# Kernel optimization log

Hardware: AMD Instinct MI355X
Metric: run time of the kernel (lower is better)

The kernel has to match this reference:

```python
import jax, jax.numpy as jnp
import numpy as np

B, I, O, ORDER = 16384, 256, 256, 8
LO, HI = -1.0, 1.0


def setup_inputs() -> dict:
    key = jax.random.key(0)
    k1, k2, k3 = jax.random.split(key, 3)
    x = jax.random.normal(k1, (B, I), dtype=jnp.float32)
    weights = jax.random.normal(k2, (O, I), dtype=jnp.float32)
    # BernsteinBasisFunction init: randn(order+1) * 0.1, one per (o, i) pair
    coeffs = jax.random.normal(k3, (O, I, ORDER + 1), dtype=jnp.float32) * 0.1
    return {"x": x, "weights": weights, "coeffs": coeffs}


def reference(x, weights, coeffs):
    # x: [B, I]; weights: [O, I]; coeffs: [O, I, K+1]
    K = coeffs.shape[-1] - 1
    zoom = (HI - LO) / 2.0
    pan = (HI + LO) / 2.0
    xt = jnp.tanh(x) * zoom + pan          # squash into [LO, HI]
    x_a = xt - LO                          # [B, I]
    x_b = HI - xt                          # [B, I]
    e = jnp.arange(K + 1)
    # ber[b, i, k] = x_a^k * x_b^(K-k)  (unnormalized Bernstein basis)
    ber = (x_a[..., None] ** e) * (x_b[..., None] ** (K - e))  # [B, I, K+1]
    # transformed[b, o, i] = sum_k coeffs[o,i,k] * ber[b,i,k]; out = einsum('boi,oi->bo')
    # Fused: fold weights into coeffs to avoid the [B, O, I] intermediate.
    wc = coeffs * weights[..., None]       # [O, I, K+1]
    return jnp.einsum('bik,oik->bo', ber, wc)
```

## Files before the change

kernel.cpp:

```cpp
#include <hip/hip_runtime.h>
#include <hip/hip_bf16.h>


#define BDIM 16384
#define IDIM 256
#define ODIM 256
#define NK 9
#define NCHUNK 4
#define NSTEP 36
#define STEP_ELEMS (ODIM * 64)
#define CGW 4

typedef short short8 __attribute__((ext_vector_type(8)));
typedef float floatx4 __attribute__((ext_vector_type(4)));

__global__ __launch_bounds__(256) void prep_wc2(const float* __restrict__ weights,
                                                const float* __restrict__ coeffs,
                                                ushort* __restrict__ wc) {
    int idx  = blockIdx.x * 256 + threadIdx.x;
    int step = idx >> 11;
    int c    = idx & 2047;
    int big    = c >> 6;
    int lane_w = c & 63;
    int o    = (big >> 1) * 16 + (lane_w & 15);
    int s    = big & 1;
    int quad = lane_w >> 4;
    int ic = step / 9;
    int k  = step - ic * 9;
    int i0 = ic * 64 + s * 32 + quad * 8;

    const float* cp = coeffs + (size_t)(o * IDIM + i0) * NK + k;
    float4 w0 = *(const float4*)(weights + o * IDIM + i0);
    float4 w1 = *(const float4*)(weights + o * IDIM + i0 + 4);
    float wv[8] = {w0.x, w0.y, w0.z, w0.w, w1.x, w1.y, w1.z, w1.w};

    union { ushort us[8]; int4 v; __hip_bfloat162 h2[4]; } pk;
#pragma unroll
    for (int j = 0; j < 8; j += 2) {
        float a = cp[(size_t)j * NK] * wv[j];
        float b = cp[(size_t)(j + 1) * NK] * wv[j + 1];
        pk.h2[j >> 1] = __float22bfloat162_rn(make_float2(a, b));
    }
    *(int4*)(wc + (size_t)step * STEP_ELEMS + (size_t)c * 8) = pk.v;
}

__global__ __launch_bounds__(512, 2) void bern_gemm(const float* __restrict__ x,
                                                    const ushort* __restrict__ wc,
                                                    float* __restrict__ out) {
    __shared__ ushort Blds[2][16384];

    const int tid  = threadIdx.x;
    const int wave = tid >> 6;
    const int lane = tid & 63;
    const int cg   = blockIdx.x & 3;
    const int rb   = (blockIdx.x >> 2) * 256 + wave * 32;
    const int lrow = lane & 15;
    const int jseg = (lane >> 4) * 8;

    float p[2][2][8];
    float r[2][2][8];
    floatx4 acc[2][4];
    floatx4 zero = {0.0f, 0.0f, 0.0f, 0.0f};
#pragma unroll
    for (int m = 0; m < 2; ++m)
#pragma unroll
        for (int n = 0; n < 4; ++n)
            acc[m][n] = zero;

#define LOAD_X(ic_)                                                             \
    {                                                                           \
        _Pragma("unroll") for (int m = 0; m < 2; ++m)                           \
        _Pragma("unroll") for (int s = 0; s < 2; ++s) {                         \
            const float* xp = x + (size_t)(rb + m * 16 + lrow) * IDIM           \
                              + (ic_) * 64 + s * 32 + jseg;                     \
            float4 v0 = *(const float4*)(xp);                                   \
            float4 v1 = *(const float4*)(xp + 4);                               \
            p[m][s][0] = v0.x; p[m][s][1] = v0.y;                               \
            p[m][s][2] = v0.z; p[m][s][3] = v0.w;                               \
            p[m][s][4] = v1.x; p[m][s][5] = v1.y;                               \
            p[m][s][6] = v1.z; p[m][s][7] = v1.w;                               \
        }                                                                       \
    }

#define SETUP_BASIS()                                                           \
    {                                                                           \
        _Pragma("unroll") for (int m = 0; m < 2; ++m)                           \
        _Pragma("unroll") for (int s = 0; s < 2; ++s)                           \
        _Pragma("unroll") for (int e = 0; e < 8; ++e) {                         \
            float t  = __builtin_amdgcn_exp2f(p[m][s][e] * 2.8853900817779268f);\
            float q  = 2.0f * __builtin_amdgcn_rcpf(t + 1.0f);                  \
            float q2 = q * q;                                                   \
            float q4 = q2 * q2;                                                 \
            p[m][s][e] = q4 * q4;                                               \
            r[m][s][e] = t;                                                     \
        }                                                                       \
    }

#define STAGE(g_, b_)                                                           \
    {                                                                           \
        _Pragma("unroll") for (int q = 0; q < 4; ++q) {                         \
            int st  = (g_) * 4 + q;                                             \
            const ushort* sp = wc + (size_t)st * STEP_ELEMS + cg * 4096         \
                               + wave * 512 + lane * 8;                         \
            ushort* dp = &Blds[b_][(q * 8 + wave) * 512 + lane * 8];            \
            __builtin_amdgcn_global_load_lds(                                   \
                (const __attribute__((address_space(1))) void*)sp,              \
                (__attribute__((address_space(3))) void*)dp, 16, 0, 0);         \
        }                                                                       \
    }

    LOAD_X(0);
    SETUP_BASIS();
    STAGE(0, 0);

#pragma unroll
    for (int g = 0; g < 9; ++g) {
        __syncthreads();
        if (g < 8) STAGE(g + 1, (g + 1) & 1);

#pragma unroll
        for (int k4 = 0; k4 < 4; ++k4) {
            const int step = g * 4 + k4;
            if (step == 9 || step == 18 || step == 27) {
                LOAD_X(step / 9);
                SETUP_BASIS();
            }
            const int kin = step % 9;

#pragma unroll
            for (int s = 0; s < 2; ++s) {
                short8 bfr[4];
#pragma unroll
                for (int n = 0; n < 4; ++n)
                    bfr[n] = *(const short8*)&Blds[g & 1]
                        [k4 * 4096 + (n * 2 + s) * 512 + lane * 8];

#pragma unroll
                for (int m = 0; m < 2; ++m) {
                    union { ushort us[8]; short8 v; __hip_bfloat162 h2[4]; } pk;
#pragma unroll
                    for (int e = 0; e < 8; e += 2) {
                        pk.h2[e >> 1] = __float22bfloat162_rn(
                            make_float2(p[m][s][e], p[m][s][e + 1]));
                    }
#pragma unroll
                    for (int n = 0; n < 4; ++n)
                        acc[m][n] = __builtin_amdgcn_mfma_f32_16x16x32_bf16(
                            pk.v, bfr[n], acc[m][n], 0, 0, 0);
                    if (kin < NK - 1)
#pragma unroll
                        for (int e = 0; e < 8; ++e) p[m][s][e] *= r[m][s][e];
                }
            }
        }
    }

#pragma unroll
    for (int m = 0; m < 2; ++m) {
#pragma unroll
        for (int n = 0; n < 4; ++n) {
            int col   = cg * 64 + n * 16 + (lane & 15);
            int rbase = rb + m * 16 + (lane >> 4) * 4;
#pragma unroll
            for (int reg = 0; reg < 4; ++reg) {
                out[(size_t)(rbase + reg) * ODIM + col] = acc[m][n][reg];
            }
        }
    }
#undef LOAD_X
#undef SETUP_BASIS
#undef STAGE
}

extern "C" void kernel_launch(void* const* d_in, const int* in_sizes, int n_in,
                              void* d_out, int out_size, void* d_ws, size_t ws_size,
                              hipStream_t stream) {
    const float* x       = (const float*)d_in[0];
    const float* weights = (const float*)d_in[1];
    const float* coeffs  = (const float*)d_in[2];
    float* out = (float*)d_out;
    ushort* wc = (ushort*)d_ws;

    prep_wc2<<<288, 256, 0, stream>>>(weights, coeffs, wc);
    bern_gemm<<<256, 512, 0, stream>>>(x, wc, out);
}
```

Measured before the change: 97.80 us.

## Restructure Bernstein GEMM into 3-step groups with prefetched x and LDS-staged prep

The main loop now runs as 12 groups of 3 k-steps, so each input chunk maps to exactly three groups and the double-buffered LDS tile shrinks to three steps. The next x chunk is prefetched into a separate register array one group early, and its basis setup is deferred until the chunk starts, which hides the global load latency behind MFMA work. The prep kernel now stages each output row's coefficients in shared memory for coalesced reads and writes scalar bf16 values. The costs are more registers, more barriers per chunk, a non-unrolled outer loop, and scattered 2-byte stores in prep.

```diff
diff --git a/kernel.cpp b/kernel.cpp
--- a/kernel.cpp
+++ b/kernel.cpp
@@ -6,48 +6,42 @@
 #define IDIM 256
 #define ODIM 256
 #define NK 9
-#define NCHUNK 4
 #define NSTEP 36
 #define STEP_ELEMS (ODIM * 64)
-#define CGW 4
+#define GSTEP 3
+#define NGROUP 12
 
 typedef short short8 __attribute__((ext_vector_type(8)));
 typedef float floatx4 __attribute__((ext_vector_type(4)));
 
-__global__ __launch_bounds__(256) void prep_wc2(const float* __restrict__ weights,
+__global__ __launch_bounds__(256) void prep_wc3(const float* __restrict__ weights,
                                                 const float* __restrict__ coeffs,
                                                 ushort* __restrict__ wc) {
-    int idx  = blockIdx.x * 256 + threadIdx.x;
-    int step = idx >> 11;
-    int c    = idx & 2047;
-    int big    = c >> 6;
-    int lane_w = c & 63;
-    int o    = (big >> 1) * 16 + (lane_w & 15);
-    int s    = big & 1;
-    int quad = lane_w >> 4;
-    int ic = step / 9;
-    int k  = step - ic * 9;
-    int i0 = ic * 64 + s * 32 + quad * 8;
+    __shared__ float cl[IDIM * NK];
+    const int o = blockIdx.x;
+    const int t = threadIdx.x;
+    const float* cb = coeffs + (size_t)o * (IDIM * NK);
+#pragma unroll
+    for (int j = 0; j < NK; ++j)
+        cl[t + 256 * j] = cb[t + 256 * j];
+    __syncthreads();
 
-    const float* cp = coeffs + (size_t)(o * IDIM + i0) * NK + k;
-    float4 w0 = *(const float4*)(weights + o * IDIM + i0);
-    float4 w1 = *(const float4*)(weights + o * IDIM + i0 + 4);
-    float wv[8] = {w0.x, w0.y, w0.z, w0.w, w1.x, w1.y, w1.z, w1.w};
-
-    union { ushort us[8]; int4 v; __hip_bfloat162 h2[4]; } pk;
+    const float wv = weights[o * IDIM + t];
+    const int ic = t >> 6, il = t & 63;
+    const int s = il >> 5, quad = (il >> 3) & 3, j = il & 7;
+    const size_t base = (size_t)((((o >> 4) * 2 + s) * 64) + (o & 15) + quad * 16) * 8 + j;
+    ushort* wb = wc + base;
 #pragma unroll
-    for (int j = 0; j < 8; j += 2) {
-        float a = cp[(size_t)j * NK] * wv[j];
-        float b = cp[(size_t)(j + 1) * NK] * wv[j + 1];
-        pk.h2[j >> 1] = __float22bfloat162_rn(make_float2(a, b));
+    for (int k = 0; k < NK; ++k) {
+        __hip_bfloat16 b = __float2bfloat16(cl[t * NK + k] * wv);
+        wb[(size_t)(ic * NK + k) * STEP_ELEMS] = *(ushort*)&b;
     }
-    *(int4*)(wc + (size_t)step * STEP_ELEMS + (size_t)c * 8) = pk.v;
 }
 
 __global__ __launch_bounds__(512, 2) void bern_gemm(const float* __restrict__ x,
                                                     const ushort* __restrict__ wc,
                                                     float* __restrict__ out) {
-    __shared__ ushort Blds[2][16384];
+    __shared__ ushort Blds[2][GSTEP * 4096];
 
     const int tid  = threadIdx.x;
     const int wave = tid >> 6;
@@ -59,6 +53,7 @@
 
     float p[2][2][8];
     float r[2][2][8];
+    float xb[2][2][8];
     floatx4 acc[2][4];
     floatx4 zero = {0.0f, 0.0f, 0.0f, 0.0f};
 #pragma unroll
@@ -75,10 +70,10 @@
                               + (ic_) * 64 + s * 32 + jseg;                     \
             float4 v0 = *(const float4*)(xp);                                   \
             float4 v1 = *(const float4*)(xp + 4);                               \
-            p[m][s][0] = v0.x; p[m][s][1] = v0.y;                               \
-            p[m][s][2] = v0.z; p[m][s][3] = v0.w;                               \
-            p[m][s][4] = v1.x; p[m][s][5] = v1.y;                               \
-            p[m][s][6] = v1.z; p[m][s][7] = v1.w;                               \
+            xb[m][s][0] = v0.x; xb[m][s][1] = v0.y;                             \
+            xb[m][s][2] = v0.z; xb[m][s][3] = v0.w;                             \
+            xb[m][s][4] = v1.x; xb[m][s][5] = v1.y;                             \
+            xb[m][s][6] = v1.z; xb[m][s][7] = v1.w;                             \
         }                                                                       \
     }
 
@@ -87,7 +82,7 @@
         _Pragma("unroll") for (int m = 0; m < 2; ++m)                           \
         _Pragma("unroll") for (int s = 0; s < 2; ++s)                           \
         _Pragma("unroll") for (int e = 0; e < 8; ++e) {                         \
-            float t  = __builtin_amdgcn_exp2f(p[m][s][e] * 2.8853900817779268f);\
+            float t  = __builtin_amdgcn_exp2f(xb[m][s][e] * 2.8853900817779268f);\
             float q  = 2.0f * __builtin_amdgcn_rcpf(t + 1.0f);                  \
             float q2 = q * q;                                                   \
             float q4 = q2 * q2;                                                 \
@@ -98,11 +93,11 @@
 
 #define STAGE(g_, b_)                                                           \
     {                                                                           \
-        _Pragma("unroll") for (int q = 0; q < 4; ++q) {                         \
-            int st  = (g_) * 4 + q;                                             \
+        _Pragma("unroll") for (int q = 0; q < GSTEP; ++q) {                     \
+            int st  = (g_) * GSTEP + q;                                         \
             const ushort* sp = wc + (size_t)st * STEP_ELEMS + cg * 4096         \
                                + wave * 512 + lane * 8;                         \
-            ushort* dp = &Blds[b_][(q * 8 + wave) * 512 + lane * 8];            \
+            ushort* dp = &Blds[b_][q * 4096 + wave * 512 + lane * 8];           \
             __builtin_amdgcn_global_load_lds(                                   \
                 (const __attribute__((address_space(1))) void*)sp,              \
                 (__attribute__((address_space(3))) void*)dp, 16, 0, 0);         \
@@ -110,48 +105,46 @@
     }
 
     LOAD_X(0);
-    SETUP_BASIS();
     STAGE(0, 0);
 
+#pragma unroll 1
+    for (int g = 0; g < NGROUP; ++g) {
+        __syncthreads();
+        if (g + 1 < NGROUP) STAGE(g + 1, (g + 1) & 1);
+
+        const int ic = g / 3;
+        const int gm = g - ic * 3;
+        if (gm == 0) SETUP_BASIS();
+        if (gm == 1 && ic + 1 < 4) LOAD_X(ic + 1);
+
+        const ushort* Bp = Blds[g & 1];
 #pragma unroll
-    for (int g = 0; g < 9; ++g) {
-        __syncthreads();
-        if (g < 8) STAGE(g + 1, (g + 1) & 1);
+        for (int q = 0; q < GSTEP; ++q) {
+            const int kc = gm * 3 + q;
+            short8 bfr[2][4];
+#pragma unroll
+            for (int s = 0; s < 2; ++s)
+#pragma unroll
+                for (int n = 0; n < 4; ++n)
+                    bfr[s][n] = *(const short8*)&Bp[q * 4096 + (n * 2 + s) * 512 + lane * 8];
 
 #pragma unroll
-        for (int k4 = 0; k4 < 4; ++k4) {
-            const int step = g * 4 + k4;
-            if (step == 9 || step == 18 || step == 27) {
-                LOAD_X(step / 9);
-                SETUP_BASIS();
-            }
-            const int kin = step % 9;
-
-#pragma unroll
-            for (int s = 0; s < 2; ++s) {
-                short8 bfr[4];
-#pragma unroll
-                for (int n = 0; n < 4; ++n)
-                    bfr[n] = *(const short8*)&Blds[g & 1]
-                        [k4 * 4096 + (n * 2 + s) * 512 + lane * 8];
-
+            for (int s = 0; s < 2; ++s)
 #pragma unroll
                 for (int m = 0; m < 2; ++m) {
-                    union { ushort us[8]; short8 v; __hip_bfloat162 h2[4]; } pk;
+                    union { short8 v; __hip_bfloat162 h2[4]; } pk;
 #pragma unroll
-                    for (int e = 0; e < 8; e += 2) {
+                    for (int e = 0; e < 8; e += 2)
                         pk.h2[e >> 1] = __float22bfloat162_rn(
                             make_float2(p[m][s][e], p[m][s][e + 1]));
-                    }
 #pragma unroll
                     for (int n = 0; n < 4; ++n)
                         acc[m][n] = __builtin_amdgcn_mfma_f32_16x16x32_bf16(
-                            pk.v, bfr[n], acc[m][n], 0, 0, 0);
-                    if (kin < NK - 1)
+                            pk.v, bfr[s][n], acc[m][n], 0, 0, 0);
+                    if (kc < NK - 1)
 #pragma unroll
                         for (int e = 0; e < 8; ++e) p[m][s][e] *= r[m][s][e];
                 }
-            }
         }
     }
 
@@ -181,6 +174,6 @@
     float* out = (float*)d_out;
     ushort* wc = (ushort*)d_ws;
 
-    prep_wc2<<<288, 256, 0, stream>>>(weights, coeffs, wc);
+    prep_wc3<<<ODIM, 256, 0, stream>>>(weights, coeffs, wc);
     bern_gemm<<<256, 512, 0, stream>>>(x, wc, out);
 }
```

Measured after the change: 105.4 us. +7.8%, slower.
